# Kernel optimization log

Hardware: AMD Instinct MI355X
Metric: run time of the kernel (lower is better)

## Reference

```python
import jax, jax.numpy as jnp
import numpy as np

SCALE = 1.0 / np.sqrt(7.0)  # window_size ** 0.5 with window_size=7


def setup_inputs() -> dict:
    key = jax.random.key(0)
    ks = jax.random.split(key, 7)
    B, C, H, W = 8, 64, 64, 64
    O = 64
    x = jax.random.normal(ks[0], (B, C, H, W), dtype=jnp.float32)
    s = 1.0 / np.sqrt(C)
    Wq = jax.random.normal(ks[1], (O, C), dtype=jnp.float32) * s
    bq = jax.random.normal(ks[2], (O,), dtype=jnp.float32) * 0.01
    Wk = jax.random.normal(ks[3], (O, C), dtype=jnp.float32) * s
    bk = jax.random.normal(ks[4], (O,), dtype=jnp.float32) * 0.01
    Wv = jax.random.normal(ks[5], (O, C), dtype=jnp.float32) * s
    bv = jax.random.normal(ks[6], (O,), dtype=jnp.float32) * 0.01
    return {"x": x, "Wq": Wq, "bq": bq, "Wk": Wk, "bk": bk, "Wv": Wv, "bv": bv}


def reference(x, Wq, bq, Wk, bk, Wv, bv):
    B, C, H, W = x.shape
    O = Wq.shape[0]
    N = H * W
    # 1x1 convs == per-pixel linear projections
    xf = x.reshape(B, C, N)  # [B, C, N]
    q = jnp.einsum('bcn,oc->bon', xf, Wq) + bq[None, :, None]  # [B, O, N]
    k = jnp.einsum('bcn,oc->bon', xf, Wk) + bk[None, :, None]
    v = jnp.einsum('bcn,oc->bon', xf, Wv) + bv[None, :, None]
    # global attention over all H*W positions
    attn = jnp.einsum('bcn,bcm->bnm', q, k) * SCALE  # [B, N, N]
    attn = jax.nn.softmax(attn, axis=-1)
    out = jnp.einsum('bnm,bcm->bnc', attn, v)  # [B, N, O]
    # faithful to torch's out.view(B, -1, H, W): raw row-major reshape of [B, N, O]
    return out.reshape(B, O, H, W)
```

## Files before the change

kernel.cpp:

```cpp
#include <hip/hip_runtime.h>
#include <math.h>

#define B_ 8
#define N_ 4096
#define SCALE2_ 0.54528747f

typedef __bf16 bf16x8 __attribute__((ext_vector_type(8)));
typedef float f32x4 __attribute__((ext_vector_type(4)));
typedef float f32x16 __attribute__((ext_vector_type(16)));
typedef unsigned short ushortx8 __attribute__((ext_vector_type(8)));
typedef unsigned short ushort;
typedef unsigned int uint;
typedef uint uint2v __attribute__((ext_vector_type(2)));

static __device__ __forceinline__ ushort f2bf(float f) {
  union { float f; unsigned u; } v; v.f = f;
  unsigned r = v.u + 0x7FFFu + ((v.u >> 16) & 1u);
  return (ushort)(r >> 16);
}
static __device__ __forceinline__ uint pk2(float a, float b) {
  union { __bf16 h[2]; uint u; } v;
  v.h[0] = (__bf16)a; v.h[1] = (__bf16)b;
  return v.u;
}

__global__ __launch_bounds__(256)
void proj_kernel(const float* __restrict__ x,
                 const float* __restrict__ Wq, const float* __restrict__ bq,
                 const float* __restrict__ Wk, const float* __restrict__ bk,
                 const float* __restrict__ Wv, const float* __restrict__ bv,
                 ushort* __restrict__ Qb, ushort* __restrict__ KF,
                 ushort* __restrict__ VF)
{
  __shared__ ushort sm[256][17];

  const int tid = threadIdx.x;
  const int gp  = (blockIdx.x << 8) + tid;
  const int b   = gp >> 12;
  const int y   = blockIdx.y;
  const int mat = y >> 2;
  const int o0  = (y & 3) << 4;
  const int n   = gp & 4095;

  const float* xb = x + ((size_t)b << 18) + n;
  float xr[64];
  #pragma unroll
  for (int c = 0; c < 64; ++c) xr[c] = xb[(size_t)c << 12];

  const float* W    = (mat == 0) ? Wq : (mat == 1) ? Wk : Wv;
  const float* bias = (mat == 0) ? bq : (mat == 1) ? bk : bv;

  float acc[16];
  #pragma unroll 1
  for (int j = 0; j < 16; ++j) {
    const float4* wr = (const float4*)(W + ((o0 + j) << 6));
    float a = bias[o0 + j];
    #pragma unroll
    for (int c4 = 0; c4 < 16; ++c4) {
      float4 w4 = wr[c4];
      a += w4.x * xr[4*c4] + w4.y * xr[4*c4+1] + w4.z * xr[4*c4+2] + w4.w * xr[4*c4+3];
    }
    acc[j] = a;
  }

  if (mat == 2) {
    #pragma unroll
    for (int j = 0; j < 16; ++j) sm[tid][j] = f2bf(acc[j]);
    __syncthreads();
    const int ol   = tid & 15;
    const int hh   = (tid >> 4) & 1;
    const int kvbl = tid >> 5;
    const int nb   = (blockIdx.x << 8) & 4095;
    const int kvblk = (nb >> 5) + kvbl;
    #pragma unroll
    for (int ks2 = 0; ks2 < 2; ++ks2) {
      const int kvl = (kvbl << 5) + (ks2 << 4) + (hh << 3);
      uint pk[4];
      #pragma unroll
      for (int cj = 0; cj < 8; ++cj) {
        ushort v = sm[kvl + cj][ol];
        if (cj & 1) pk[cj >> 1] |= (uint)v << 16; else pk[cj >> 1] = v;
      }
      const size_t A = ((size_t)(b * 128 + kvblk)) * 2048 + (ks2 << 10)
                     + (hh << 9) + ((o0 + ol) << 3);
      *(ushortx8*)(VF + A) = *(ushortx8*)&pk[0];
    }
  } else if (mat == 1) {
    const int ks = y & 3;
    __align__(16) ushort hv[16];
    #pragma unroll
    for (int j = 0; j < 16; ++j) hv[j] = f2bf(acc[j]);
    const size_t A0 = ((size_t)(b * 128 + (n >> 5))) * 2048 + (ks << 9)
                    + ((n & 31) << 3);
    *(ushortx8*)(KF + A0)       = *(const ushortx8*)&hv[0];
    *(ushortx8*)(KF + A0 + 256) = *(const ushortx8*)&hv[8];
  } else {
    __align__(16) ushort hv[16];
    #pragma unroll
    for (int j = 0; j < 16; ++j) hv[j] = f2bf(acc[j] * SCALE2_);
    const size_t base = ((size_t)gp << 6) + o0;
    *(ushortx8*)(Qb + base)     = *(const ushortx8*)&hv[0];
    *(ushortx8*)(Qb + base + 8) = *(const ushortx8*)&hv[8];
  }
}

__global__ __launch_bounds__(256, 2)
void flash_kernel(const ushort* __restrict__ Qb, const ushort* __restrict__ KF,
                  const ushort* __restrict__ VF, float* __restrict__ out)
{
  __shared__ float cmb[3][64][66];

  const int tid  = threadIdx.x;
  const int lane = tid & 63;
  const int w    = tid >> 6;
  const int r32  = lane & 31;
  const int h    = lane >> 5;
  const int h8   = h << 3;

  const int bidx = (blockIdx.x & 7) * 64 + (blockIdx.x >> 3);
  const int b  = bidx >> 6;
  const int qw = (bidx & 63) << 6;

  bf16x8 qfA[4], qfB[4];
  {
    const ushort* qa = Qb + ((((size_t)b << 12) + qw + r32) << 6) + h8;
    const ushort* qb2 = Qb + ((((size_t)b << 12) + qw + 32 + r32) << 6) + h8;
    #pragma unroll
    for (int ks = 0; ks < 4; ++ks) {
      qfA[ks] = *(const bf16x8*)(qa + (ks << 4));
      qfB[ks] = *(const bf16x8*)(qb2 + (ks << 4));
    }
  }

  const ushort* kb = KF + ((size_t)((b << 7) + (w << 5))) * 2048 + (lane << 3);
  const ushort* vb = VF + ((size_t)((b << 7) + (w << 5))) * 2048 + (h << 9) + (r32 << 3);

  const f32x16 Z = (f32x16)(0.0f);
  f32x16 accA0 = Z, accA1 = Z, accB0 = Z, accB1 = Z;
  float lA = 0.f, lB = 0.f;

  #define TILE(QF, A0, A1, LV) do { \
    __builtin_amdgcn_s_setprio(1); \
    f32x16 s = __builtin_amdgcn_mfma_f32_32x32x16_bf16(k0, QF[0], Z, 0, 0, 0); \
    s = __builtin_amdgcn_mfma_f32_32x32x16_bf16(k1, QF[1], s, 0, 0, 0); \
    s = __builtin_amdgcn_mfma_f32_32x32x16_bf16(k2, QF[2], s, 0, 0, 0); \
    s = __builtin_amdgcn_mfma_f32_32x32x16_bf16(k3, QF[3], s, 0, 0, 0); \
    __builtin_amdgcn_s_setprio(0); \
    float rs = 0.f; \
    _Pragma("unroll") \
    for (int ii = 0; ii < 16; ++ii) { \
      float p = __builtin_exp2f(s[ii]); \
      s[ii] = p; \
      rs += p; \
    } \
    LV += rs; \
    bf16x8 pb0, pb1; \
    { \
      uint plo0 = pk2(s[0], s[1]); \
      uint plo1 = pk2(s[2], s[3]); \
      uint phi0 = pk2(s[4], s[5]); \
      uint phi1 = pk2(s[6], s[7]); \
      uint2v r0 = __builtin_amdgcn_permlane32_swap(plo0, phi0, false, false); \
      uint2v r1 = __builtin_amdgcn_permlane32_swap(plo1, phi1, false, false); \
      union { uint u[4]; bf16x8 v; } f_; \
      f_.u[0] = r0.x; f_.u[1] = r1.x; f_.u[2] = r0.y; f_.u[3] = r1.y; \
      pb0 = f_.v; \
    } \
    { \
      uint plo0 = pk2(s[8],  s[9]); \
      uint plo1 = pk2(s[10], s[11]); \
      uint phi0 = pk2(s[12], s[13]); \
      uint phi1 = pk2(s[14], s[15]); \
      uint2v r0 = __builtin_amdgcn_permlane32_swap(plo0, phi0, false, false); \
      uint2v r1 = __builtin_amdgcn_permlane32_swap(plo1, phi1, false, false); \
      union { uint u[4]; bf16x8 v; } f_; \
      f_.u[0] = r0.x; f_.u[1] = r1.x; f_.u[2] = r0.y; f_.u[3] = r1.y; \
      pb1 = f_.v; \
    } \
    __builtin_amdgcn_s_setprio(1); \
    A0 = __builtin_amdgcn_mfma_f32_32x32x16_bf16(v0, pb0, A0, 0, 0, 0); \
    A1 = __builtin_amdgcn_mfma_f32_32x32x16_bf16(v1, pb0, A1, 0, 0, 0); \
    A0 = __builtin_amdgcn_mfma_f32_32x32x16_bf16(v2, pb1, A0, 0, 0, 0); \
    A1 = __builtin_amdgcn_mfma_f32_32x32x16_bf16(v3, pb1, A1, 0, 0, 0); \
    __builtin_amdgcn_s_setprio(0); \
  } while (0)

  #pragma unroll 1
  for (int t = 0; t < 32; ++t) {
    bf16x8 k0 = *(const bf16x8*)(kb);
    bf16x8 k1 = *(const bf16x8*)(kb + 512);
    bf16x8 k2 = *(const bf16x8*)(kb + 1024);
    bf16x8 k3 = *(const bf16x8*)(kb + 1536);
    bf16x8 v0 = *(const bf16x8*)(vb);
    bf16x8 v1 = *(const bf16x8*)(vb + 256);
    bf16x8 v2 = *(const bf16x8*)(vb + 1024);
    bf16x8 v3 = *(const bf16x8*)(vb + 1280);
    kb += 2048; vb += 2048;

    TILE(qfA, accA0, accA1, lA);
    TILE(qfB, accB0, accB1, lB);
  }
  #undef TILE

  float lAm = lA + __shfl_xor(lA, 32);
  float lBm = lB + __shfl_xor(lB, 32);

  if (w != 0) {
    float* p = &cmb[w - 1][lane][0];
    #pragma unroll
    for (int i = 0; i < 16; ++i) {
      p[i]      = accA0[i];
      p[16 + i] = accA1[i];
      p[32 + i] = accB0[i];
      p[48 + i] = accB1[i];
    }
    p[64] = lAm;
    p[65] = lBm;
  }
  __syncthreads();
  if (w == 0) {
    float lsA = lAm, lsB = lBm;
    #pragma unroll
    for (int q = 0; q < 3; ++q) { lsA += cmb[q][lane][64]; lsB += cmb[q][lane][65]; }
    const float invA = 1.0f / lsA;
    const float invB = 1.0f / lsB;
    const size_t rowA = (((size_t)b << 12) + qw + r32) << 6;
    const size_t rowB = (((size_t)b << 12) + qw + 32 + r32) << 6;
    #pragma unroll
    for (int g = 0; g < 4; ++g) {
      f32x4 oA, oB;
      #pragma unroll
      for (int i = 0; i < 4; ++i) {
        float vA0 = accA0[4*g + i], vB0 = accB0[4*g + i];
        #pragma unroll
        for (int q = 0; q < 3; ++q) {
          vA0 += cmb[q][lane][4*g + i];
          vB0 += cmb[q][lane][32 + 4*g + i];
        }
        oA[i] = vA0 * invA;
        oB[i] = vB0 * invB;
      }
      *(f32x4*)(out + rowA + (g << 3) + (h << 2)) = oA;
      *(f32x4*)(out + rowB + (g << 3) + (h << 2)) = oB;
    }
    #pragma unroll
    for (int g = 0; g < 4; ++g) {
      f32x4 oA, oB;
      #pragma unroll
      for (int i = 0; i < 4; ++i) {
        float vA1 = accA1[4*g + i], vB1 = accB1[4*g + i];
        #pragma unroll
        for (int q = 0; q < 3; ++q) {
          vA1 += cmb[q][lane][16 + 4*g + i];
          vB1 += cmb[q][lane][48 + 4*g + i];
        }
        oA[i] = vA1 * invA;
        oB[i] = vB1 * invB;
      }
      *(f32x4*)(out + rowA + 32 + (g << 3) + (h << 2)) = oA;
      *(f32x4*)(out + rowB + 32 + (g << 3) + (h << 2)) = oB;
    }
  }
}

extern "C" void kernel_launch(void* const* d_in, const int* in_sizes, int n_in,
                              void* d_out, int out_size, void* d_ws, size_t ws_size,
                              hipStream_t stream) {
  (void)in_sizes; (void)n_in; (void)out_size; (void)ws_size;
  const float* x  = (const float*)d_in[0];
  const float* Wq = (const float*)d_in[1];
  const float* bq = (const float*)d_in[2];
  const float* Wk = (const float*)d_in[3];
  const float* bk = (const float*)d_in[4];
  const float* Wv = (const float*)d_in[5];
  const float* bv = (const float*)d_in[6];
  float* out = (float*)d_out;

  const size_t SZ = (size_t)B_ * N_ * 64;
  ushort* Qb = (ushort*)d_ws;
  ushort* KF = Qb + SZ;
  ushort* VF = KF + SZ;

  proj_kernel<<<dim3(128, 12), dim3(256), 0, stream>>>(x, Wq, bq, Wk, bk, Wv, bv,
                                                       Qb, KF, VF);
  flash_kernel<<<dim3(512), dim3(256), 0, stream>>>(Qb, KF, VF, out);
}
```

Baseline: 80.65 us.

## Compute QKV projections with bf16 MFMA using split hi/lo inputs

Rewrites the projection kernel to use 32x32x16 bf16 MFMA instructions instead of scalar FP32 FMAs. The input x is split into high and low bf16 parts to recover precision, and outputs are rearranged with permlane32 swaps to write directly into the fragment layouts that the flash kernel expects. This removes the shared-memory transpose for V. The grid changes so that each block computes all 64 output channels for 128 pixels, so x is loaded once per matrix rather than once per 16-channel slice. The weights are rounded to bf16, which loses some accuracy.

```diff
diff --git a/kernel.cpp b/kernel.cpp
--- a/kernel.cpp
+++ b/kernel.cpp
@@ -17,6 +17,10 @@
   union { float f; unsigned u; } v; v.f = f;
   unsigned r = v.u + 0x7FFFu + ((v.u >> 16) & 1u);
   return (ushort)(r >> 16);
+}
+static __device__ __forceinline__ float bf2f(ushort h) {
+  union { unsigned u; float f; } v; v.u = ((unsigned)h) << 16;
+  return v.f;
 }
 static __device__ __forceinline__ uint pk2(float a, float b) {
   union { __bf16 h[2]; uint u; } v;
@@ -32,75 +36,111 @@
                  ushort* __restrict__ Qb, ushort* __restrict__ KF,
                  ushort* __restrict__ VF)
 {
-  __shared__ ushort sm[256][17];
-
-  const int tid = threadIdx.x;
-  const int gp  = (blockIdx.x << 8) + tid;
-  const int b   = gp >> 12;
-  const int y   = blockIdx.y;
-  const int mat = y >> 2;
-  const int o0  = (y & 3) << 4;
-  const int n   = gp & 4095;
-
-  const float* xb = x + ((size_t)b << 18) + n;
-  float xr[64];
-  #pragma unroll
-  for (int c = 0; c < 64; ++c) xr[c] = xb[(size_t)c << 12];
+  const int tid  = threadIdx.x;
+  const int lane = tid & 63;
+  const int w    = tid >> 6;
+  const int r32  = lane & 31;
+  const int h2   = lane >> 5;
+  const int mat  = blockIdx.y;
+
+  const int gp0 = blockIdx.x << 7;
+  const int b   = gp0 >> 12;
+  const int nb  = gp0 & 4095;
+  const int n   = nb + (w << 5) + r32;
 
   const float* W    = (mat == 0) ? Wq : (mat == 1) ? Wk : Wv;
   const float* bias = (mat == 0) ? bq : (mat == 1) ? bk : bv;
-
-  float acc[16];
-  #pragma unroll 1
-  for (int j = 0; j < 16; ++j) {
-    const float4* wr = (const float4*)(W + ((o0 + j) << 6));
-    float a = bias[o0 + j];
-    #pragma unroll
-    for (int c4 = 0; c4 < 16; ++c4) {
-      float4 w4 = wr[c4];
-      a += w4.x * xr[4*c4] + w4.y * xr[4*c4+1] + w4.z * xr[4*c4+2] + w4.w * xr[4*c4+3];
-    }
-    acc[j] = a;
-  }
-
-  if (mat == 2) {
-    #pragma unroll
-    for (int j = 0; j < 16; ++j) sm[tid][j] = f2bf(acc[j]);
-    __syncthreads();
-    const int ol   = tid & 15;
-    const int hh   = (tid >> 4) & 1;
-    const int kvbl = tid >> 5;
-    const int nb   = (blockIdx.x << 8) & 4095;
-    const int kvblk = (nb >> 5) + kvbl;
-    #pragma unroll
-    for (int ks2 = 0; ks2 < 2; ++ks2) {
-      const int kvl = (kvbl << 5) + (ks2 << 4) + (hh << 3);
-      uint pk[4];
-      #pragma unroll
-      for (int cj = 0; cj < 8; ++cj) {
-        ushort v = sm[kvl + cj][ol];
-        if (cj & 1) pk[cj >> 1] |= (uint)v << 16; else pk[cj >> 1] = v;
-      }
-      const size_t A = ((size_t)(b * 128 + kvblk)) * 2048 + (ks2 << 10)
-                     + (hh << 9) + ((o0 + ol) << 3);
-      *(ushortx8*)(VF + A) = *(ushortx8*)&pk[0];
-    }
-  } else if (mat == 1) {
-    const int ks = y & 3;
-    __align__(16) ushort hv[16];
-    #pragma unroll
-    for (int j = 0; j < 16; ++j) hv[j] = f2bf(acc[j]);
-    const size_t A0 = ((size_t)(b * 128 + (n >> 5))) * 2048 + (ks << 9)
-                    + ((n & 31) << 3);
-    *(ushortx8*)(KF + A0)       = *(const ushortx8*)&hv[0];
-    *(ushortx8*)(KF + A0 + 256) = *(const ushortx8*)&hv[8];
-  } else {
-    __align__(16) ushort hv[16];
-    #pragma unroll
-    for (int j = 0; j < 16; ++j) hv[j] = f2bf(acc[j] * SCALE2_);
-    const size_t base = ((size_t)gp << 6) + o0;
-    *(ushortx8*)(Qb + base)     = *(const ushortx8*)&hv[0];
-    *(ushortx8*)(Qb + base + 8) = *(const ushortx8*)&hv[8];
+  const float  scl  = (mat == 0) ? SCALE2_ : 1.0f;
+
+  bf16x8 xh[4], xl[4];
+  #pragma unroll
+  for (int ks = 0; ks < 4; ++ks) {
+    union { ushort u[8]; bf16x8 v; } th, tl;
+    #pragma unroll
+    for (int j = 0; j < 8; ++j) {
+      const int c = (ks << 4) + (h2 << 3) + j;
+      float val = x[((size_t)b << 18) + ((size_t)c << 12) + n];
+      ushort hv = f2bf(val);
+      th.u[j] = hv;
+      tl.u[j] = f2bf(val - bf2f(hv));
+    }
+    xh[ks] = th.v;
+    xl[ks] = tl.v;
+  }
+
+  bf16x8 wf[2][4];
+  #pragma unroll
+  for (int t = 0; t < 2; ++t) {
+    #pragma unroll
+    for (int ks = 0; ks < 4; ++ks) {
+      const float* wp = W + (((t << 5) + r32) << 6) + (ks << 4) + (h2 << 3);
+      float4 a  = *(const float4*)wp;
+      float4 c4 = *(const float4*)(wp + 4);
+      union { ushort u[8]; bf16x8 v; } tw;
+      tw.u[0] = f2bf(a.x * scl);  tw.u[1] = f2bf(a.y * scl);
+      tw.u[2] = f2bf(a.z * scl);  tw.u[3] = f2bf(a.w * scl);
+      tw.u[4] = f2bf(c4.x * scl); tw.u[5] = f2bf(c4.y * scl);
+      tw.u[6] = f2bf(c4.z * scl); tw.u[7] = f2bf(c4.w * scl);
+      wf[t][ks] = tw.v;
+    }
+  }
+
+  const f32x16 Z = (f32x16)(0.0f);
+  const size_t rowb = (((size_t)b << 12) + n) << 6;
+  const size_t kfb  = ((size_t)(b * 128 + (nb >> 5) + w)) * 2048;
+
+  #pragma unroll
+  for (int t = 0; t < 2; ++t) {
+    f32x16 Dh = Z, Dl = Z;
+    if (mat == 2) {
+      #pragma unroll
+      for (int ks = 0; ks < 4; ++ks) {
+        Dh = __builtin_amdgcn_mfma_f32_32x32x16_bf16(xh[ks], wf[t][ks], Dh, 0, 0, 0);
+        Dl = __builtin_amdgcn_mfma_f32_32x32x16_bf16(xl[ks], wf[t][ks], Dl, 0, 0, 0);
+      }
+    } else {
+      #pragma unroll
+      for (int ks = 0; ks < 4; ++ks) {
+        Dh = __builtin_amdgcn_mfma_f32_32x32x16_bf16(wf[t][ks], xh[ks], Dh, 0, 0, 0);
+        Dl = __builtin_amdgcn_mfma_f32_32x32x16_bf16(wf[t][ks], xl[ks], Dl, 0, 0, 0);
+      }
+    }
+
+    f32x16 D;
+    if (mat == 2) {
+      const float bvl = bias[(t << 5) + r32];
+      #pragma unroll
+      for (int i = 0; i < 16; ++i) D[i] = Dh[i] + Dl[i] + bvl;
+    } else {
+      float bm[16];
+      #pragma unroll
+      for (int g2 = 0; g2 < 4; ++g2) {
+        float4 t4 = *(const float4*)(bias + (t << 5) + (g2 << 3) + (h2 << 2));
+        bm[4*g2+0] = t4.x * scl; bm[4*g2+1] = t4.y * scl;
+        bm[4*g2+2] = t4.z * scl; bm[4*g2+3] = t4.w * scl;
+      }
+      #pragma unroll
+      for (int i = 0; i < 16; ++i) D[i] = Dh[i] + Dl[i] + bm[i];
+    }
+
+    #pragma unroll
+    for (int g = 0; g < 2; ++g) {
+      uint plo0 = pk2(D[8*g+0], D[8*g+1]);
+      uint plo1 = pk2(D[8*g+2], D[8*g+3]);
+      uint phi0 = pk2(D[8*g+4], D[8*g+5]);
+      uint phi1 = pk2(D[8*g+6], D[8*g+7]);
+      uint2v r0 = __builtin_amdgcn_permlane32_swap(plo0, phi0, false, false);
+      uint2v r1 = __builtin_amdgcn_permlane32_swap(plo1, phi1, false, false);
+      union { uint u[4]; ushortx8 v8; } ch;
+      ch.u[0] = r0.x; ch.u[1] = r1.x; ch.u[2] = r0.y; ch.u[3] = r1.y;
+      if (mat == 0) {
+        *(ushortx8*)(Qb + rowb + (t << 5) + (g << 4) + (h2 << 3)) = ch.v8;
+      } else if (mat == 1) {
+        *(ushortx8*)(KF + kfb + ((2*t + g) << 9) + (h2 << 8) + (r32 << 3)) = ch.v8;
+      } else {
+        *(ushortx8*)(VF + kfb + (g << 10) + (h2 << 9) + (((t << 5) + r32) << 3)) = ch.v8;
+      }
+    }
   }
 }
 
@@ -281,7 +321,7 @@
   ushort* KF = Qb + SZ;
   ushort* VF = KF + SZ;
 
-  proj_kernel<<<dim3(128, 12), dim3(256), 0, stream>>>(x, Wq, bq, Wk, bk, Wv, bv,
-                                                       Qb, KF, VF);
+  proj_kernel<<<dim3(256, 3), dim3(256), 0, stream>>>(x, Wq, bq, Wk, bk, Wv, bv,
+                                                      Qb, KF, VF);
   flash_kernel<<<dim3(512), dim3(256), 0, stream>>>(Qb, KF, VF, out);
 }
```

Result: faster. 72.00 us (median of 2 runs) (-10.7%).
